# Optimization experiments

Hardware: AMD Instinct MI355X
Metric: run time of the kernel (lower is better)

Reference implementation:

```python
import jax, jax.numpy as jnp
import numpy as np

IN_DIM = 256
OUT_DIM = 256
NUM = 5        # grid_size
K = 3          # spline_order
GRID_RANGE = (-1.0, 1.0)


def extend_grid(grid, k_extend):
    # grid: (in_dim, num+1) -> (in_dim, num+1+2*k_extend)
    h = (grid[:, -1:] - grid[:, :1]) / (grid.shape[1] - 1)
    for _ in range(k_extend):
        grid = jnp.concatenate([grid[:, :1] - h, grid, grid[:, -1:] + h], axis=1)
    return grid


def b_spline_basis(x, grid, k):
    # x: (B, in_dim), grid: (in_dim, G). Cox-de Boor recursion, vectorized.
    x = x[:, :, None]                 # (B, in, 1)
    g = grid[None, :, :]              # (1, in, G)
    B = ((x >= g[:, :, :-1]) & (x < g[:, :, 1:])).astype(x.dtype)  # order 0
    for p in range(1, k + 1):
        left = (x - g[:, :, :-(p + 1)]) / (g[:, :, p:-1] - g[:, :, :-(p + 1)])
        right = (g[:, :, p + 1:] - x) / (g[:, :, p + 1:] - g[:, :, 1:-p])
        B = left * B[:, :, :-1] + right * B[:, :, 1:]
    return jnp.nan_to_num(B)          # (B, in, num+k)


def setup_inputs() -> dict:
    key = jax.random.key(0)
    kx, kc, kb, ks = jax.random.split(key, 4)
    x = jax.random.uniform(kx, (2048, IN_DIM), dtype=jnp.float32,
                           minval=GRID_RANGE[0], maxval=GRID_RANGE[1])
    base_grid = jnp.broadcast_to(
        jnp.linspace(GRID_RANGE[0], GRID_RANGE[1], NUM + 1, dtype=jnp.float32)[None, :],
        (IN_DIM, NUM + 1))
    grid = extend_grid(base_grid, K)                        # (in, num+1+2k)
    coef = 0.1 * jax.random.normal(kc, (IN_DIM, OUT_DIM, NUM + K), dtype=jnp.float32)
    scale_base = ((jax.random.uniform(kb, (IN_DIM, OUT_DIM), dtype=jnp.float32) * 2 - 1)
                  / np.sqrt(IN_DIM).astype(np.float32))
    scale_sp = jnp.ones((IN_DIM, OUT_DIM), dtype=jnp.float32)
    mask = jnp.ones((IN_DIM, OUT_DIM), dtype=jnp.float32)
    return {"x": x, "grid": grid, "coef": coef,
            "scale_base": scale_base, "scale_sp": scale_sp, "mask": mask}


def reference(x, grid, coef, scale_base, scale_sp, mask):
    base = jax.nn.silu(x)                                   # (B, in)
    B = b_spline_basis(x, grid, K)                          # (B, in, num+k)
    # coef2curve: (B, in, G) x (in, out, G) -> (B, in, out)
    y = jnp.einsum('big,iog->bio', B, coef)
    y = scale_base[None, :, :] * base[:, :, None] + scale_sp[None, :, :] * y
    y = mask[None, :, :] * y
    return jnp.sum(y, axis=1)                               # (B, out)
```

## Files before the change

### kernel.cpp

```cpp
#include <hip/hip_runtime.h>

#define BATCH 2048
#define IND   256
#define OUTD  256

typedef __attribute__((ext_vector_type(8))) short bf16x8;
typedef __attribute__((ext_vector_type(4))) float f32x4;

__device__ __forceinline__ ushort f2bf(float f) {
    uint u = __builtin_bit_cast(uint, f);
    u += 0x7fffu + ((u >> 16) & 1u);
    return (ushort)(u >> 16);
}
__device__ __forceinline__ uint pack2(float lo, float hi) {
    return (uint)f2bf(lo) | ((uint)f2bf(hi) << 16);
}

#define BIASOFF (1u << 20)
#define FOFF    ((1u << 20) + 4096)
#define WS_NEED ((size_t)FOFF + (size_t)IND * BATCH * 16)

__device__ __forceinline__ uint4 feat_pack(float xv) {
    const float u = (xv + 1.0f) * 2.5f;
    float cif = floorf(u);
    cif = fminf(fmaxf(cif, 0.0f), 4.0f);
    const int ci = (int)cif;
    const float f = u - cif, mf = 1.0f - f;
    const float f2 = f * f, f3 = f2 * f;
    const float k6 = 1.0f / 6.0f;
    const float w0 = mf * mf * mf * k6;
    const float w1 = (3.0f * f3 - 6.0f * f2 + 4.0f) * k6;
    const float w3 = f3 * k6;
    const float w2 = 1.0f - w0 - w1 - w3;
    const float sg = __fdividef(xv, 1.0f + __expf(-xv));
    const float B0 = (ci == 0) ? w0 : 0.f;
    const float B1 = (ci == 1) ? w0 : (ci == 0) ? w1 : 0.f;
    const float B2 = (ci == 2) ? w0 : (ci == 1) ? w1 : (ci == 0) ? w2 : 0.f;
    const float B3 = (ci == 3) ? w0 : (ci == 2) ? w1 : (ci == 1) ? w2 : (ci == 0) ? w3 : 0.f;
    const float B4 = (ci == 4) ? w0 : (ci == 3) ? w1 : (ci == 2) ? w2 : (ci == 1) ? w3 : 0.f;
    const float B5 = (ci == 4) ? w1 : (ci == 3) ? w2 : (ci == 2) ? w3 : 0.f;
    const float B6 = (ci == 4) ? w2 : (ci == 3) ? w3 : 0.f;
    uint4 v;
    v.x = pack2(sg, B0); v.y = pack2(B1, B2);
    v.z = pack2(B3, B4); v.w = pack2(B5, B6);
    return v;
}

__global__ __launch_bounds__(256) void kan_prep(
    const float* __restrict__ x, const float* __restrict__ coef,
    const float* __restrict__ sb, const float* __restrict__ ss,
    const float* __restrict__ mask,
    uint4* __restrict__ W, float* __restrict__ bias, uint4* __restrict__ F)
{
    const int bid = blockIdx.x, tid = threadIdx.x;
    __shared__ float xt[4 * 260];
    __shared__ float part[32][8];

    const int b0 = (bid & 7) * 256 + (bid >> 3) * 4;
    {
        const int row = tid >> 6, c4 = (tid & 63) * 4;
        const float4 v = *reinterpret_cast<const float4*>(
            x + (size_t)(b0 + row) * IND + c4);
        xt[row * 260 + c4 + 0] = v.x;
        xt[row * 260 + c4 + 1] = v.y;
        xt[row * 260 + c4 + 2] = v.z;
        xt[row * 260 + c4 + 3] = v.w;
    }

    if (tid < 128) {
        const int i = bid >> 1, o = (bid & 1) * 128 + tid;
        const int io = i * OUTD + o;
        const float m = mask[io], b = sb[io], sp = ss[io];
        const float4* cp = reinterpret_cast<const float4*>(coef + (size_t)io * 8);
        const float4 c0 = cp[0], c1 = cp[1];
        const float wb = m * b, wsp = m * sp;
        const float c7 = c1.w;
        uint4 w;
        w.x = pack2(wb,                wsp * (c0.x - c7));
        w.y = pack2(wsp * (c0.y - c7), wsp * (c0.z - c7));
        w.z = pack2(wsp * (c0.w - c7), wsp * (c1.x - c7));
        w.w = pack2(wsp * (c1.y - c7), wsp * (c1.z - c7));
        W[io] = w;
    }
    __syncthreads();

#pragma unroll
    for (int p = 0; p < 4; ++p) {
        const int q = p * 256 + tid;
        const int i = q >> 2, b = q & 3;
        F[(size_t)i * BATCH + b0 + b] = feat_pack(xt[b * 260 + i]);
    }

    if (bid >= 480) {
        const int o0 = (bid - 480) * 8;
        const int ol = tid & 7, ig = tid >> 3;
        float s = 0.f;
#pragma unroll
        for (int ii = 0; ii < 8; ++ii) {
            const int i = ig * 8 + ii;
            const int io = i * OUTD + o0 + ol;
            s += mask[io] * ss[io] * coef[(size_t)io * 8 + 7];
        }
        part[ig][ol] = s;
        __syncthreads();
        if (tid < 8) {
            float acc = 0.f;
#pragma unroll
            for (int g2 = 0; g2 < 32; ++g2) acc += part[g2][tid];
            bias[o0 + tid] = acc;
        }
    }
}

__global__ __launch_bounds__(512, 4) void kan_gemm(
    const uint4* __restrict__ F, const uint4* __restrict__ W,
    const float* __restrict__ bias, float* __restrict__ out)
{
    const int tid  = threadIdx.x;
    const int lane = tid & 63, wid = tid >> 6;
    const int nh = wid & 1, kq = wid >> 1;
    const int r = lane & 15, g = lane >> 4;
    const int bid = blockIdx.x;
    const int q = bid >> 3;
    const int b0 = ((bid & 7) * 8 + (q >> 2)) * 32;
    const int o0 = (q & 3) * 64;

    const uint4* pA = F + (size_t)(kq * 64 + g) * BATCH + b0 + r;
    const uint4* pB = W + (size_t)(kq * 64 + g) * OUTD + o0 + nh * 32 + r;

    f32x4 acc[2][2] = {};
    bf16x8 a0_0, a1_0, b0_0, b1_0;
    bf16x8 a0_1, a1_1, b0_1, b1_1;
    bf16x8 a0_2, a1_2, b0_2, b1_2;
    bf16x8 a0_3, a1_3, b0_3, b1_3;

#define LDS_(s, t)                                                                     \
    {                                                                                  \
        a0_##s = *reinterpret_cast<const bf16x8*>(pA + (size_t)(4 * (t)) * BATCH);     \
        a1_##s = *reinterpret_cast<const bf16x8*>(pA + (size_t)(4 * (t)) * BATCH + 16);\
        b0_##s = *reinterpret_cast<const bf16x8*>(pB + (size_t)(4 * (t)) * OUTD);      \
        b1_##s = *reinterpret_cast<const bf16x8*>(pB + (size_t)(4 * (t)) * OUTD + 16); \
    }
#define MM_(s)                                                                         \
    {                                                                                  \
        acc[0][0] = __builtin_amdgcn_mfma_f32_16x16x32_bf16(a0_##s, b0_##s, acc[0][0], 0, 0, 0); \
        acc[0][1] = __builtin_amdgcn_mfma_f32_16x16x32_bf16(a0_##s, b1_##s, acc[0][1], 0, 0, 0); \
        acc[1][0] = __builtin_amdgcn_mfma_f32_16x16x32_bf16(a1_##s, b0_##s, acc[1][0], 0, 0, 0); \
        acc[1][1] = __builtin_amdgcn_mfma_f32_16x16x32_bf16(a1_##s, b1_##s, acc[1][1], 0, 0, 0); \
    }

    LDS_(0, 0)  LDS_(1, 1)  LDS_(2, 2)  LDS_(3, 3)
    MM_(0) LDS_(0, 4)   MM_(1) LDS_(1, 5)   MM_(2) LDS_(2, 6)   MM_(3) LDS_(3, 7)
    MM_(0) LDS_(0, 8)   MM_(1) LDS_(1, 9)   MM_(2) LDS_(2, 10)  MM_(3) LDS_(3, 11)
    MM_(0) LDS_(0, 12)  MM_(1) LDS_(1, 13)  MM_(2) LDS_(2, 14)  MM_(3) LDS_(3, 15)
    MM_(0) MM_(1) MM_(2) MM_(3)
#undef LDS_
#undef MM_

    __shared__ float red[2][3][1024];
    if (kq > 0) {
        float* dst = &red[nh][kq - 1][0];
#pragma unroll
        for (int mf = 0; mf < 2; ++mf)
#pragma unroll
            for (int nf = 0; nf < 2; ++nf)
                *reinterpret_cast<f32x4*>(dst + (mf * 2 + nf) * 256 + lane * 4) = acc[mf][nf];
    }
    __syncthreads();
    if (kq == 0) {
#pragma unroll
        for (int mf = 0; mf < 2; ++mf)
#pragma unroll
            for (int nf = 0; nf < 2; ++nf) {
                f32x4 s = acc[mf][nf];
                const int sl = (mf * 2 + nf) * 256 + lane * 4;
#pragma unroll
                for (int kk = 0; kk < 3; ++kk) {
                    const f32x4 v = *reinterpret_cast<const f32x4*>(&red[nh][kk][0] + sl);
                    s.x += v.x; s.y += v.y; s.z += v.z; s.w += v.w;
                }
                const int col  = o0 + nh * 32 + nf * 16 + r;
                const int row0 = b0 + mf * 16 + g * 4;
                const float bv = bias[col];
#pragma unroll
                for (int e = 0; e < 4; ++e)
                    out[(size_t)(row0 + e) * OUTD + col] = s[e] + bv;
            }
    }
}

#define KPI  16
#define IPC  8
#define KC   (IPC * KPI)

__global__ __launch_bounds__(256, 2) void kan_mfma(
    const float* __restrict__ x, const float* __restrict__ coef,
    const float* __restrict__ scale_base, const float* __restrict__ scale_sp,
    const float* __restrict__ mask, float* __restrict__ out)
{
    const int tid = threadIdx.x;
    const int b0 = blockIdx.x * 32, o0 = blockIdx.y * 32;
    __shared__ uint Fa[32 * KC / 2];
    __shared__ uint Wt2[32 * KC / 2];
    for (int j = tid; j < 32 * KC / 2; j += 256) { Fa[j] = 0u; Wt2[j] = 0u; }
    const int lane = tid & 63, wid = tid >> 6;
    const int wmv = (wid >> 1) * 16, wnv = (wid & 1) * 16;
    f32x4 acc = {0.f, 0.f, 0.f, 0.f};
    const int fb = tid & 31, il = tid >> 5;
    for (int ic = 0; ic < IND / IPC; ++ic) {
        const int i = ic * IPC + il;
        __syncthreads();
        {
            const uint4 fp = feat_pack(x[(b0 + fb) * IND + i]);
            const int base = fb * (KC / 2) + il * (KPI / 2);
            const int sw = (fb & 7) << 2;
            Fa[(base + 0) ^ sw] = fp.x; Fa[(base + 1) ^ sw] = fp.y;
            Fa[(base + 2) ^ sw] = fp.z; Fa[(base + 3) ^ sw] = fp.w;
            ((ushort*)Fa)[2 * ((base + 4) ^ sw)] = 0;
        }
        {
            const int io = i * OUTD + o0 + fb;
            const float m = mask[io];
            const float wb = scale_base[io] * m, wsv = scale_sp[io] * m;
            const float4* cp = reinterpret_cast<const float4*>(coef + (size_t)io * 8);
            const float4 c0 = cp[0], c1 = cp[1];
            const float c7 = c1.w;
            const int base = fb * (KC / 2) + il * (KPI / 2);
            const int sw = (fb & 7) << 2;
            Wt2[(base + 0) ^ sw] = pack2(wb, wsv * (c0.x - c7));
            Wt2[(base + 1) ^ sw] = pack2(wsv * (c0.y - c7), wsv * (c0.z - c7));
            Wt2[(base + 2) ^ sw] = pack2(wsv * (c0.w - c7), wsv * (c1.x - c7));
            Wt2[(base + 3) ^ sw] = pack2(wsv * (c1.y - c7), wsv * (c1.z - c7));
            ((ushort*)Wt2)[2 * ((base + 4) ^ sw)] = 0;
        }
        __syncthreads();
        {
            const ushort* fs = (const ushort*)Fa;
            const ushort* wsd = (const ushort*)Wt2;
            const int ar = wmv + (lane & 15), br = wnv + (lane & 15);
            const int kg = (lane >> 4) * 8;
#pragma unroll
            for (int ksi = 0; ksi < 4; ++ksi) {
                const int ka = ksi * 32 + kg;
                const int ia = (ar * KC + ka) ^ ((ar & 7) << 3);
                const int ib = (br * KC + ka) ^ ((br & 7) << 3);
                bf16x8 a = *reinterpret_cast<const bf16x8*>(fs + ia);
                bf16x8 b = *reinterpret_cast<const bf16x8*>(wsd + ib);
                acc = __builtin_amdgcn_mfma_f32_16x16x32_bf16(a, b, acc, 0, 0, 0);
            }
        }
    }
    const int col = o0 + wnv + (lane & 15);
    const int row0 = b0 + wmv + ((lane >> 4) << 2);
    float bv = 0.f;
    for (int i = 0; i < IND; ++i) {
        const int io = i * OUTD + col;
        bv += mask[io] * scale_sp[io] * coef[(size_t)io * 8 + 7];
    }
#pragma unroll
    for (int rr = 0; rr < 4; ++rr)
        out[(size_t)(row0 + rr) * OUTD + col] = acc[rr] + bv;
}

extern "C" void kernel_launch(void* const* d_in, const int* in_sizes, int n_in,
                              void* d_out, int out_size, void* d_ws, size_t ws_size,
                              hipStream_t stream) {
    const float* x          = (const float*)d_in[0];
    const float* coef       = (const float*)d_in[2];
    const float* scale_base = (const float*)d_in[3];
    const float* scale_sp   = (const float*)d_in[4];
    const float* mask       = (const float*)d_in[5];
    float* out = (float*)d_out;

    if (ws_size >= WS_NEED) {
        uint4* W    = (uint4*)d_ws;
        float* bias = (float*)((char*)d_ws + BIASOFF);
        uint4* F    = (uint4*)((char*)d_ws + FOFF);
        kan_prep<<<512, 256, 0, stream>>>(x, coef, scale_base, scale_sp, mask, W, bias, F);
        kan_gemm<<<256, 512, 0, stream>>>(F, W, bias, out);
    } else {
        kan_mfma<<<dim3(BATCH / 32, OUTD / 32), 256, 0, stream>>>(
            x, coef, scale_base, scale_sp, mask, out);
    }
}
```

Baseline: 18.27 us.

## Fuse B-spline feature computation into GEMM kernel, drop feature workspace

The B-spline and SiLU feature packing moves out of the prep kernel and into the GEMM kernel. Each block stages its 32 rows of x in shared memory, computes bf16 features per K-chunk into a swizzled LDS tile, and feeds them to MFMA. This removes the 8 MB feature buffer write and re-read through global memory, and the prep kernel now only builds weights and bias. In exchange the GEMM recomputes features four times, once per output-column block, and adds two barriers per K-step, which reduces load/compute overlap compared with the previous register-pipelined loads.

```diff
diff --git a/kernel.cpp b/kernel.cpp
--- a/kernel.cpp
+++ b/kernel.cpp
@@ -17,8 +17,7 @@
 }
 
 #define BIASOFF (1u << 20)
-#define FOFF    ((1u << 20) + 4096)
-#define WS_NEED ((size_t)FOFF + (size_t)IND * BATCH * 16)
+#define WS_NEED ((size_t)BIASOFF + 4096)
 
 __device__ __forceinline__ uint4 feat_pack(float xv) {
     const float u = (xv + 1.0f) * 2.5f;
@@ -46,30 +45,15 @@
     return v;
 }
 
-__global__ __launch_bounds__(256) void kan_prep(
-    const float* __restrict__ x, const float* __restrict__ coef,
-    const float* __restrict__ sb, const float* __restrict__ ss,
-    const float* __restrict__ mask,
-    uint4* __restrict__ W, float* __restrict__ bias, uint4* __restrict__ F)
+__global__ __launch_bounds__(256) void kan_wb(
+    const float* __restrict__ coef, const float* __restrict__ sb,
+    const float* __restrict__ ss, const float* __restrict__ mask,
+    uint4* __restrict__ W, float* __restrict__ bias)
 {
     const int bid = blockIdx.x, tid = threadIdx.x;
-    __shared__ float xt[4 * 260];
     __shared__ float part[32][8];
-
-    const int b0 = (bid & 7) * 256 + (bid >> 3) * 4;
-    {
-        const int row = tid >> 6, c4 = (tid & 63) * 4;
-        const float4 v = *reinterpret_cast<const float4*>(
-            x + (size_t)(b0 + row) * IND + c4);
-        xt[row * 260 + c4 + 0] = v.x;
-        xt[row * 260 + c4 + 1] = v.y;
-        xt[row * 260 + c4 + 2] = v.z;
-        xt[row * 260 + c4 + 3] = v.w;
-    }
-
-    if (tid < 128) {
-        const int i = bid >> 1, o = (bid & 1) * 128 + tid;
-        const int io = i * OUTD + o;
+    if (bid < 256) {
+        const int io = bid * OUTD + tid;
         const float m = mask[io], b = sb[io], sp = ss[io];
         const float4* cp = reinterpret_cast<const float4*>(coef + (size_t)io * 8);
         const float4 c0 = cp[0], c1 = cp[1];
@@ -81,18 +65,8 @@
         w.z = pack2(wsp * (c0.w - c7), wsp * (c1.x - c7));
         w.w = pack2(wsp * (c1.y - c7), wsp * (c1.z - c7));
         W[io] = w;
-    }
-    __syncthreads();
-
-#pragma unroll
-    for (int p = 0; p < 4; ++p) {
-        const int q = p * 256 + tid;
-        const int i = q >> 2, b = q & 3;
-        F[(size_t)i * BATCH + b0 + b] = feat_pack(xt[b * 260 + i]);
-    }
-
-    if (bid >= 480) {
-        const int o0 = (bid - 480) * 8;
+    } else {
+        const int o0 = (bid - 256) * 8;
         const int ol = tid & 7, ig = tid >> 3;
         float s = 0.f;
 #pragma unroll
@@ -112,54 +86,78 @@
     }
 }
 
-__global__ __launch_bounds__(512, 4) void kan_gemm(
-    const uint4* __restrict__ F, const uint4* __restrict__ W,
+__global__ __launch_bounds__(512, 4) void kan_fgemm(
+    const float* __restrict__ x, const uint4* __restrict__ W,
     const float* __restrict__ bias, float* __restrict__ out)
 {
+    __shared__ float xs[32 * 256];
+    __shared__ uint4 At[32 * 32];
+
     const int tid  = threadIdx.x;
     const int lane = tid & 63, wid = tid >> 6;
     const int nh = wid & 1, kq = wid >> 1;
     const int r = lane & 15, g = lane >> 4;
     const int bid = blockIdx.x;
-    const int q = bid >> 3;
-    const int b0 = ((bid & 7) * 8 + (q >> 2)) * 32;
-    const int o0 = (q & 3) * 64;
-
-    const uint4* pA = F + (size_t)(kq * 64 + g) * BATCH + b0 + r;
-    const uint4* pB = W + (size_t)(kq * 64 + g) * OUTD + o0 + nh * 32 + r;
+    const int xcd = bid & 7;
+    const int o0 = (xcd >> 1) * 64;
+    const int b0 = ((bid >> 3) * 2 + (xcd & 1)) * 32;
+
+    {
+        const int row = tid >> 4, c0 = (tid & 15) * 4;
+#pragma unroll
+        for (int q2 = 0; q2 < 4; ++q2) {
+            const float4 v = *reinterpret_cast<const float4*>(
+                x + (size_t)(b0 + row) * IND + c0 + q2 * 64);
+            *reinterpret_cast<float4*>(xs + row * 256 + c0 + q2 * 64) = v;
+        }
+    }
+
+    const int frow = tid >> 5;
+    const int fil  = tid & 31;
 
     f32x4 acc[2][2] = {};
-    bf16x8 a0_0, a1_0, b0_0, b1_0;
-    bf16x8 a0_1, a1_1, b0_1, b1_1;
-    bf16x8 a0_2, a1_2, b0_2, b1_2;
-    bf16x8 a0_3, a1_3, b0_3, b1_3;
-
-#define LDS_(s, t)                                                                     \
-    {                                                                                  \
-        a0_##s = *reinterpret_cast<const bf16x8*>(pA + (size_t)(4 * (t)) * BATCH);     \
-        a1_##s = *reinterpret_cast<const bf16x8*>(pA + (size_t)(4 * (t)) * BATCH + 16);\
-        b0_##s = *reinterpret_cast<const bf16x8*>(pB + (size_t)(4 * (t)) * OUTD);      \
-        b1_##s = *reinterpret_cast<const bf16x8*>(pB + (size_t)(4 * (t)) * OUTD + 16); \
-    }
-#define MM_(s)                                                                         \
-    {                                                                                  \
-        acc[0][0] = __builtin_amdgcn_mfma_f32_16x16x32_bf16(a0_##s, b0_##s, acc[0][0], 0, 0, 0); \
-        acc[0][1] = __builtin_amdgcn_mfma_f32_16x16x32_bf16(a0_##s, b1_##s, acc[0][1], 0, 0, 0); \
-        acc[1][0] = __builtin_amdgcn_mfma_f32_16x16x32_bf16(a1_##s, b0_##s, acc[1][0], 0, 0, 0); \
-        acc[1][1] = __builtin_amdgcn_mfma_f32_16x16x32_bf16(a1_##s, b1_##s, acc[1][1], 0, 0, 0); \
-    }
-
-    LDS_(0, 0)  LDS_(1, 1)  LDS_(2, 2)  LDS_(3, 3)
-    MM_(0) LDS_(0, 4)   MM_(1) LDS_(1, 5)   MM_(2) LDS_(2, 6)   MM_(3) LDS_(3, 7)
-    MM_(0) LDS_(0, 8)   MM_(1) LDS_(1, 9)   MM_(2) LDS_(2, 10)  MM_(3) LDS_(3, 11)
-    MM_(0) LDS_(0, 12)  MM_(1) LDS_(1, 13)  MM_(2) LDS_(2, 14)  MM_(3) LDS_(3, 15)
-    MM_(0) MM_(1) MM_(2) MM_(3)
-#undef LDS_
-#undef MM_
-
-    __shared__ float red[2][3][1024];
+    __syncthreads();
+
+#pragma unroll
+    for (int t = 0; t < 8; ++t) {
+        const int i0 = t * 32;
+
+        const uint4* pB = W + (size_t)(i0 + kq * 8 + g) * OUTD + o0 + nh * 32 + r;
+        const bf16x8 b00 = *reinterpret_cast<const bf16x8*>(pB);
+        const bf16x8 b01 = *reinterpret_cast<const bf16x8*>(pB + 16);
+        const bf16x8 b10 = *reinterpret_cast<const bf16x8*>(pB + 4 * OUTD);
+        const bf16x8 b11 = *reinterpret_cast<const bf16x8*>(pB + 4 * OUTD + 16);
+
+        const uint4 f0 = feat_pack(xs[frow * 256 + i0 + fil]);
+        const uint4 f1 = feat_pack(xs[(frow + 16) * 256 + i0 + fil]);
+
+        __syncthreads();
+        At[frow * 32 + (fil ^ (frow & 7))] = f0;
+        At[(frow + 16) * 32 + (fil ^ ((frow + 16) & 7))] = f1;
+        __syncthreads();
+
+        const int s0 = kq * 8 + g;
+        const int s1 = s0 + 4;
+        const int ra0 = r, ra1 = 16 + r;
+        const bf16x8 a00 = *reinterpret_cast<const bf16x8*>(At + ra0 * 32 + (s0 ^ (ra0 & 7)));
+        const bf16x8 a10 = *reinterpret_cast<const bf16x8*>(At + ra1 * 32 + (s0 ^ (ra1 & 7)));
+        const bf16x8 a01 = *reinterpret_cast<const bf16x8*>(At + ra0 * 32 + (s1 ^ (ra0 & 7)));
+        const bf16x8 a11 = *reinterpret_cast<const bf16x8*>(At + ra1 * 32 + (s1 ^ (ra1 & 7)));
+
+        acc[0][0] = __builtin_amdgcn_mfma_f32_16x16x32_bf16(a00, b00, acc[0][0], 0, 0, 0);
+        acc[0][1] = __builtin_amdgcn_mfma_f32_16x16x32_bf16(a00, b01, acc[0][1], 0, 0, 0);
+        acc[1][0] = __builtin_amdgcn_mfma_f32_16x16x32_bf16(a10, b00, acc[1][0], 0, 0, 0);
+        acc[1][1] = __builtin_amdgcn_mfma_f32_16x16x32_bf16(a10, b01, acc[1][1], 0, 0, 0);
+        acc[0][0] = __builtin_amdgcn_mfma_f32_16x16x32_bf16(a01, b10, acc[0][0], 0, 0, 0);
+        acc[0][1] = __builtin_amdgcn_mfma_f32_16x16x32_bf16(a01, b11, acc[0][1], 0, 0, 0);
+        acc[1][0] = __builtin_amdgcn_mfma_f32_16x16x32_bf16(a11, b10, acc[1][0], 0, 0, 0);
+        acc[1][1] = __builtin_amdgcn_mfma_f32_16x16x32_bf16(a11, b11, acc[1][1], 0, 0, 0);
+    }
+
+    __syncthreads();
+    float* red = xs;
     if (kq > 0) {
-        float* dst = &red[nh][kq - 1][0];
+        float* dst = red + (size_t)(nh * 3 + kq - 1) * 1024;
 #pragma unroll
         for (int mf = 0; mf < 2; ++mf)
 #pragma unroll
@@ -176,7 +174,8 @@
                 const int sl = (mf * 2 + nf) * 256 + lane * 4;
 #pragma unroll
                 for (int kk = 0; kk < 3; ++kk) {
-                    const f32x4 v = *reinterpret_cast<const f32x4*>(&red[nh][kk][0] + sl);
+                    const f32x4 v = *reinterpret_cast<const f32x4*>(
+                        red + (size_t)(nh * 3 + kk) * 1024 + sl);
                     s.x += v.x; s.y += v.y; s.z += v.z; s.w += v.w;
                 }
                 const int col  = o0 + nh * 32 + nf * 16 + r;
@@ -275,9 +274,8 @@
     if (ws_size >= WS_NEED) {
         uint4* W    = (uint4*)d_ws;
         float* bias = (float*)((char*)d_ws + BIASOFF);
-        uint4* F    = (uint4*)((char*)d_ws + FOFF);
-        kan_prep<<<512, 256, 0, stream>>>(x, coef, scale_base, scale_sp, mask, W, bias, F);
-        kan_gemm<<<256, 512, 0, stream>>>(F, W, bias, out);
+        kan_wb<<<288, 256, 0, stream>>>(coef, scale_base, scale_sp, mask, W, bias);
+        kan_fgemm<<<256, 512, 0, stream>>>(x, W, bias, out);
     } else {
         kan_mfma<<<dim3(BATCH / 32, OUTD / 32), 256, 0, stream>>>(
             x, coef, scale_base, scale_sp, mask, out);
```

Result: slower. 18.93 us (+3.6%).

## Halve GEMM output tile to 32x32 and double grid to 512 blocks

Applied to the files above, without the earlier changes.

The GEMM block tile shrinks from 32 batch x 64 outputs to 32x32, with the two wave halves now splitting batch rows instead of output columns, and the launch grows to 512 blocks. Each wave does two MFMAs per k-step instead of four, and the LDS reduction buffer is halved. This spreads the work over more CUs and waves on a small problem. In exchange each block reuses its loaded A and B tiles less, so total global loads go up.

```diff
diff --git a/kernel.cpp b/kernel.cpp
--- a/kernel.cpp
+++ b/kernel.cpp
@@ -118,35 +118,32 @@
 {
     const int tid  = threadIdx.x;
     const int lane = tid & 63, wid = tid >> 6;
-    const int nh = wid & 1, kq = wid >> 1;
+    const int mh = wid & 1, kq = wid >> 1;
     const int r = lane & 15, g = lane >> 4;
     const int bid = blockIdx.x;
-    const int q = bid >> 3;
-    const int b0 = ((bid & 7) * 8 + (q >> 2)) * 32;
-    const int o0 = (q & 3) * 64;
-
-    const uint4* pA = F + (size_t)(kq * 64 + g) * BATCH + b0 + r;
-    const uint4* pB = W + (size_t)(kq * 64 + g) * OUTD + o0 + nh * 32 + r;
-
-    f32x4 acc[2][2] = {};
-    bf16x8 a0_0, a1_0, b0_0, b1_0;
-    bf16x8 a0_1, a1_1, b0_1, b1_1;
-    bf16x8 a0_2, a1_2, b0_2, b1_2;
-    bf16x8 a0_3, a1_3, b0_3, b1_3;
+    const int xcd = bid & 7, rest = bid >> 3;
+    const int b0 = (xcd * 8 + (rest >> 3)) * 32;
+    const int o0 = (rest & 7) * 32;
+
+    const uint4* pA = F + (size_t)(kq * 64 + g) * BATCH + b0 + mh * 16 + r;
+    const uint4* pB = W + (size_t)(kq * 64 + g) * OUTD + o0 + r;
+
+    f32x4 acc[2] = {};
+    bf16x8 a_0, b0_0, b1_0;
+    bf16x8 a_1, b0_1, b1_1;
+    bf16x8 a_2, b0_2, b1_2;
+    bf16x8 a_3, b0_3, b1_3;
 
 #define LDS_(s, t)                                                                     \
     {                                                                                  \
-        a0_##s = *reinterpret_cast<const bf16x8*>(pA + (size_t)(4 * (t)) * BATCH);     \
-        a1_##s = *reinterpret_cast<const bf16x8*>(pA + (size_t)(4 * (t)) * BATCH + 16);\
+        a_##s  = *reinterpret_cast<const bf16x8*>(pA + (size_t)(4 * (t)) * BATCH);     \
         b0_##s = *reinterpret_cast<const bf16x8*>(pB + (size_t)(4 * (t)) * OUTD);      \
         b1_##s = *reinterpret_cast<const bf16x8*>(pB + (size_t)(4 * (t)) * OUTD + 16); \
     }
 #define MM_(s)                                                                         \
     {                                                                                  \
-        acc[0][0] = __builtin_amdgcn_mfma_f32_16x16x32_bf16(a0_##s, b0_##s, acc[0][0], 0, 0, 0); \
-        acc[0][1] = __builtin_amdgcn_mfma_f32_16x16x32_bf16(a0_##s, b1_##s, acc[0][1], 0, 0, 0); \
-        acc[1][0] = __builtin_amdgcn_mfma_f32_16x16x32_bf16(a1_##s, b0_##s, acc[1][0], 0, 0, 0); \
-        acc[1][1] = __builtin_amdgcn_mfma_f32_16x16x32_bf16(a1_##s, b1_##s, acc[1][1], 0, 0, 0); \
+        acc[0] = __builtin_amdgcn_mfma_f32_16x16x32_bf16(a_##s, b0_##s, acc[0], 0, 0, 0); \
+        acc[1] = __builtin_amdgcn_mfma_f32_16x16x32_bf16(a_##s, b1_##s, acc[1], 0, 0, 0); \
     }
 
     LDS_(0, 0)  LDS_(1, 1)  LDS_(2, 2)  LDS_(3, 3)
@@ -157,35 +154,31 @@
 #undef LDS_
 #undef MM_
 
-    __shared__ float red[2][3][1024];
+    __shared__ float red[2][3][512];
     if (kq > 0) {
-        float* dst = &red[nh][kq - 1][0];
-#pragma unroll
-        for (int mf = 0; mf < 2; ++mf)
-#pragma unroll
-            for (int nf = 0; nf < 2; ++nf)
-                *reinterpret_cast<f32x4*>(dst + (mf * 2 + nf) * 256 + lane * 4) = acc[mf][nf];
+        float* dst = &red[mh][kq - 1][0];
+#pragma unroll
+        for (int nf = 0; nf < 2; ++nf)
+            *reinterpret_cast<f32x4*>(dst + nf * 256 + lane * 4) = acc[nf];
     }
     __syncthreads();
     if (kq == 0) {
 #pragma unroll
-        for (int mf = 0; mf < 2; ++mf)
-#pragma unroll
-            for (int nf = 0; nf < 2; ++nf) {
-                f32x4 s = acc[mf][nf];
-                const int sl = (mf * 2 + nf) * 256 + lane * 4;
-#pragma unroll
-                for (int kk = 0; kk < 3; ++kk) {
-                    const f32x4 v = *reinterpret_cast<const f32x4*>(&red[nh][kk][0] + sl);
-                    s.x += v.x; s.y += v.y; s.z += v.z; s.w += v.w;
-                }
-                const int col  = o0 + nh * 32 + nf * 16 + r;
-                const int row0 = b0 + mf * 16 + g * 4;
-                const float bv = bias[col];
-#pragma unroll
-                for (int e = 0; e < 4; ++e)
-                    out[(size_t)(row0 + e) * OUTD + col] = s[e] + bv;
+        for (int nf = 0; nf < 2; ++nf) {
+            f32x4 s = acc[nf];
+            const int sl = nf * 256 + lane * 4;
+#pragma unroll
+            for (int kk = 0; kk < 3; ++kk) {
+                const f32x4 v = *reinterpret_cast<const f32x4*>(&red[mh][kk][0] + sl);
+                s.x += v.x; s.y += v.y; s.z += v.z; s.w += v.w;
             }
+            const int col  = o0 + nf * 16 + r;
+            const int row0 = b0 + mh * 16 + g * 4;
+            const float bv = bias[col];
+#pragma unroll
+            for (int e = 0; e < 4; ++e)
+                out[(size_t)(row0 + e) * OUTD + col] = s[e] + bv;
+        }
     }
 }
 
@@ -277,7 +270,7 @@
         float* bias = (float*)((char*)d_ws + BIASOFF);
         uint4* F    = (uint4*)((char*)d_ws + FOFF);
         kan_prep<<<512, 256, 0, stream>>>(x, coef, scale_base, scale_sp, mask, W, bias, F);
-        kan_gemm<<<256, 512, 0, stream>>>(F, W, bias, out);
+        kan_gemm<<<512, 512, 0, stream>>>(F, W, bias, out);
     } else {
         kan_mfma<<<dim3(BATCH / 32, OUTD / 32), 256, 0, stream>>>(
             x, coef, scale_base, scale_sp, mask, out);
```

Result: slower. 18.75 us (+2.6%).

## Stage full-K weight slice in 128KB LDS and retile GEMM to 64x32

Applied to the files above, without the earlier changes.

The GEMM kernel now copies the whole 256x32 weight slice for its output columns into 128KB of dynamic shared memory (XOR-swizzled), then streams the feature operand from global memory with a one-step register prefetch. Block tiling changes from 32 batch x 64 out to 64 batch x 32 out, and the split-K reduction buffer reuses the same LDS. The aim is to cut repeated global weight reads and raise reuse per block. The cost is one block per CU, the up-front staging latency before any MFMA runs, and a hipFuncSetAttribute call on every launch.

```diff
diff --git a/kernel.cpp b/kernel.cpp
--- a/kernel.cpp
+++ b/kernel.cpp
@@ -19,6 +19,8 @@
 #define BIASOFF (1u << 20)
 #define FOFF    ((1u << 20) + 4096)
 #define WS_NEED ((size_t)FOFF + (size_t)IND * BATCH * 16)
+
+#define LDSB2   131072
 
 __device__ __forceinline__ uint4 feat_pack(float xv) {
     const float u = (xv + 1.0f) * 2.5f;
@@ -46,6 +48,18 @@
     return v;
 }
 
+__device__ __forceinline__ uint4 wpack(float m, float b, float sp,
+                                       float4 c0, float4 c1) {
+    const float wb = m * b, wsp = m * sp;
+    const float c7 = c1.w;
+    uint4 w;
+    w.x = pack2(wb,                wsp * (c0.x - c7));
+    w.y = pack2(wsp * (c0.y - c7), wsp * (c0.z - c7));
+    w.z = pack2(wsp * (c0.w - c7), wsp * (c1.x - c7));
+    w.w = pack2(wsp * (c1.y - c7), wsp * (c1.z - c7));
+    return w;
+}
+
 __global__ __launch_bounds__(256) void kan_prep(
     const float* __restrict__ x, const float* __restrict__ coef,
     const float* __restrict__ sb, const float* __restrict__ ss,
@@ -66,31 +80,19 @@
         xt[row * 260 + c4 + 2] = v.z;
         xt[row * 260 + c4 + 3] = v.w;
     }
-
     if (tid < 128) {
         const int i = bid >> 1, o = (bid & 1) * 128 + tid;
         const int io = i * OUTD + o;
-        const float m = mask[io], b = sb[io], sp = ss[io];
         const float4* cp = reinterpret_cast<const float4*>(coef + (size_t)io * 8);
-        const float4 c0 = cp[0], c1 = cp[1];
-        const float wb = m * b, wsp = m * sp;
-        const float c7 = c1.w;
-        uint4 w;
-        w.x = pack2(wb,                wsp * (c0.x - c7));
-        w.y = pack2(wsp * (c0.y - c7), wsp * (c0.z - c7));
-        w.z = pack2(wsp * (c0.w - c7), wsp * (c1.x - c7));
-        w.w = pack2(wsp * (c1.y - c7), wsp * (c1.z - c7));
-        W[io] = w;
-    }
-    __syncthreads();
-
+        W[io] = wpack(mask[io], sb[io], ss[io], cp[0], cp[1]);
+    }
+    __syncthreads();
 #pragma unroll
     for (int p = 0; p < 4; ++p) {
         const int q = p * 256 + tid;
         const int i = q >> 2, b = q & 3;
         F[(size_t)i * BATCH + b0 + b] = feat_pack(xt[b * 260 + i]);
     }
-
     if (bid >= 480) {
         const int o0 = (bid - 480) * 8;
         const int ol = tid & 7, ig = tid >> 3;
@@ -112,54 +114,60 @@
     }
 }
 
-__global__ __launch_bounds__(512, 4) void kan_gemm(
+__global__ __launch_bounds__(512, 1) void kan_gemm(
     const uint4* __restrict__ F, const uint4* __restrict__ W,
     const float* __restrict__ bias, float* __restrict__ out)
 {
+    extern __shared__ uint4 Wl[];
+
     const int tid  = threadIdx.x;
     const int lane = tid & 63, wid = tid >> 6;
-    const int nh = wid & 1, kq = wid >> 1;
+    const int mh = wid & 1, kq = wid >> 1;
     const int r = lane & 15, g = lane >> 4;
     const int bid = blockIdx.x;
-    const int q = bid >> 3;
-    const int b0 = ((bid & 7) * 8 + (q >> 2)) * 32;
-    const int o0 = (q & 3) * 64;
-
-    const uint4* pA = F + (size_t)(kq * 64 + g) * BATCH + b0 + r;
-    const uint4* pB = W + (size_t)(kq * 64 + g) * OUTD + o0 + nh * 32 + r;
-
+    const int xcd = bid & 7;
+    const int b0 = xcd * 256 + ((bid >> 3) & 3) * 64;
+    const int o0 = (bid >> 5) * 32;
+
+#pragma unroll
+    for (int p = 0; p < 16; ++p) {
+        const int s = p * 512 + tid;
+        const int i = s >> 5, o = s & 31;
+        Wl[i * 32 + (o ^ (i & 7))] = W[(size_t)i * OUTD + o0 + o];
+    }
+    __syncthreads();
+
+    const int rowA0 = b0 + mh * 32 + r;
     f32x4 acc[2][2] = {};
-    bf16x8 a0_0, a1_0, b0_0, b1_0;
-    bf16x8 a0_1, a1_1, b0_1, b1_1;
-    bf16x8 a0_2, a1_2, b0_2, b1_2;
-    bf16x8 a0_3, a1_3, b0_3, b1_3;
-
-#define LDS_(s, t)                                                                     \
-    {                                                                                  \
-        a0_##s = *reinterpret_cast<const bf16x8*>(pA + (size_t)(4 * (t)) * BATCH);     \
-        a1_##s = *reinterpret_cast<const bf16x8*>(pA + (size_t)(4 * (t)) * BATCH + 16);\
-        b0_##s = *reinterpret_cast<const bf16x8*>(pB + (size_t)(4 * (t)) * OUTD);      \
-        b1_##s = *reinterpret_cast<const bf16x8*>(pB + (size_t)(4 * (t)) * OUTD + 16); \
-    }
-#define MM_(s)                                                                         \
-    {                                                                                  \
-        acc[0][0] = __builtin_amdgcn_mfma_f32_16x16x32_bf16(a0_##s, b0_##s, acc[0][0], 0, 0, 0); \
-        acc[0][1] = __builtin_amdgcn_mfma_f32_16x16x32_bf16(a0_##s, b1_##s, acc[0][1], 0, 0, 0); \
-        acc[1][0] = __builtin_amdgcn_mfma_f32_16x16x32_bf16(a1_##s, b0_##s, acc[1][0], 0, 0, 0); \
-        acc[1][1] = __builtin_amdgcn_mfma_f32_16x16x32_bf16(a1_##s, b1_##s, acc[1][1], 0, 0, 0); \
-    }
-
-    LDS_(0, 0)  LDS_(1, 1)  LDS_(2, 2)  LDS_(3, 3)
-    MM_(0) LDS_(0, 4)   MM_(1) LDS_(1, 5)   MM_(2) LDS_(2, 6)   MM_(3) LDS_(3, 7)
-    MM_(0) LDS_(0, 8)   MM_(1) LDS_(1, 9)   MM_(2) LDS_(2, 10)  MM_(3) LDS_(3, 11)
-    MM_(0) LDS_(0, 12)  MM_(1) LDS_(1, 13)  MM_(2) LDS_(2, 14)  MM_(3) LDS_(3, 15)
-    MM_(0) MM_(1) MM_(2) MM_(3)
-#undef LDS_
-#undef MM_
-
-    __shared__ float red[2][3][1024];
+
+    const uint4* pA = F + (size_t)(kq * 64 + g) * BATCH + rowA0;
+    bf16x8 aC0 = *reinterpret_cast<const bf16x8*>(pA);
+    bf16x8 aC1 = *reinterpret_cast<const bf16x8*>(pA + 16);
+    bf16x8 aN0, aN1;
+
+#pragma unroll
+    for (int t = 0; t < 16; ++t) {
+        const int i = kq * 64 + t * 4 + g;
+        if (t < 15) {
+            const uint4* pn = F + (size_t)(i + 4) * BATCH + rowA0;
+            aN0 = *reinterpret_cast<const bf16x8*>(pn);
+            aN1 = *reinterpret_cast<const bf16x8*>(pn + 16);
+        }
+        const bf16x8 bb0 = __builtin_bit_cast(bf16x8, Wl[i * 32 + (r ^ (i & 7))]);
+        const bf16x8 bb1 = __builtin_bit_cast(bf16x8, Wl[i * 32 + ((16 + r) ^ (i & 7))]);
+
+        acc[0][0] = __builtin_amdgcn_mfma_f32_16x16x32_bf16(aC0, bb0, acc[0][0], 0, 0, 0);
+        acc[0][1] = __builtin_amdgcn_mfma_f32_16x16x32_bf16(aC0, bb1, acc[0][1], 0, 0, 0);
+        acc[1][0] = __builtin_amdgcn_mfma_f32_16x16x32_bf16(aC1, bb0, acc[1][0], 0, 0, 0);
+        acc[1][1] = __builtin_amdgcn_mfma_f32_16x16x32_bf16(aC1, bb1, acc[1][1], 0, 0, 0);
+
+        aC0 = aN0; aC1 = aN1;
+    }
+
+    __syncthreads();
+    float* red = (float*)Wl;
     if (kq > 0) {
-        float* dst = &red[nh][kq - 1][0];
+        float* dst = red + (size_t)(mh * 3 + kq - 1) * 1024;
 #pragma unroll
         for (int mf = 0; mf < 2; ++mf)
 #pragma unroll
@@ -176,11 +184,12 @@
                 const int sl = (mf * 2 + nf) * 256 + lane * 4;
 #pragma unroll
                 for (int kk = 0; kk < 3; ++kk) {
-                    const f32x4 v = *reinterpret_cast<const f32x4*>(&red[nh][kk][0] + sl);
+                    const f32x4 v = *reinterpret_cast<const f32x4*>(
+                        red + (size_t)(mh * 3 + kk) * 1024 + sl);
                     s.x += v.x; s.y += v.y; s.z += v.z; s.w += v.w;
                 }
-                const int col  = o0 + nh * 32 + nf * 16 + r;
-                const int row0 = b0 + mf * 16 + g * 4;
+                const int col  = o0 + nf * 16 + r;
+                const int row0 = b0 + mh * 32 + mf * 16 + g * 4;
                 const float bv = bias[col];
 #pragma unroll
                 for (int e = 0; e < 4; ++e)
@@ -220,17 +229,14 @@
         }
         {
             const int io = i * OUTD + o0 + fb;
-            const float m = mask[io];
-            const float wb = scale_base[io] * m, wsv = scale_sp[io] * m;
             const float4* cp = reinterpret_cast<const float4*>(coef + (size_t)io * 8);
-            const float4 c0 = cp[0], c1 = cp[1];
-            const float c7 = c1.w;
+            const uint4 w = wpack(mask[io], scale_base[io], scale_sp[io], cp[0], cp[1]);
             const int base = fb * (KC / 2) + il * (KPI / 2);
             const int sw = (fb & 7) << 2;
-            Wt2[(base + 0) ^ sw] = pack2(wb, wsv * (c0.x - c7));
-            Wt2[(base + 1) ^ sw] = pack2(wsv * (c0.y - c7), wsv * (c0.z - c7));
-            Wt2[(base + 2) ^ sw] = pack2(wsv * (c0.w - c7), wsv * (c1.x - c7));
-            Wt2[(base + 3) ^ sw] = pack2(wsv * (c1.y - c7), wsv * (c1.z - c7));
+            Wt2[(base + 0) ^ sw] = w.x;
+            Wt2[(base + 1) ^ sw] = w.y;
+            Wt2[(base + 2) ^ sw] = w.z;
+            Wt2[(base + 3) ^ sw] = w.w;
             ((ushort*)Wt2)[2 * ((base + 4) ^ sw)] = 0;
         }
         __syncthreads();
@@ -272,12 +278,15 @@
     const float* mask       = (const float*)d_in[5];
     float* out = (float*)d_out;
 
-    if (ws_size >= WS_NEED) {
+    hipError_t e = hipFuncSetAttribute(
+        (const void*)kan_gemm, hipFuncAttributeMaxDynamicSharedMemorySize, LDSB2);
+
+    if (e == hipSuccess && ws_size >= WS_NEED) {
         uint4* W    = (uint4*)d_ws;
         float* bias = (float*)((char*)d_ws + BIASOFF);
         uint4* F    = (uint4*)((char*)d_ws + FOFF);
         kan_prep<<<512, 256, 0, stream>>>(x, coef, scale_base, scale_sp, mask, W, bias, F);
-        kan_gemm<<<256, 512, 0, stream>>>(F, W, bias, out);
+        kan_gemm<<<256, 512, LDSB2, stream>>>(F, W, bias, out);
     } else {
         kan_mfma<<<dim3(BATCH / 32, OUTD / 32), 256, 0, stream>>>(
             x, coef, scale_base, scale_sp, mask, out);
```

Measured after the change: 17.39 us. -4.9%, faster.
